# Kernel tuning notes

Measured on AMD Instinct MI355X. Metric: run time of the kernel, lower is better.

## Reference

```python
import jax, jax.numpy as jnp
import numpy as np

SIGMA = 0.01        # config['fscore_sigma']
FSCORE_W = 0.1      # config['fscore_weight']
TASK_W = 1.0        # config['task_weight']
DOMAIN_W = 0.1      # config['domain_weight']


def setup_inputs() -> dict:
    key = jax.random.key(0)
    ks = jax.random.split(key, 11)
    B, N, M, F = 8, 4096, 4096, 512
    H1, H2, D = 256, 128, 6
    return {
        "pred_pc": jax.random.normal(ks[0], (B, N, 3), jnp.float32),
        "target_pc": jax.random.normal(ks[1], (B, M, 3), jnp.float32),
        "domain_features": jax.random.normal(ks[2], (B, F), jnp.float32),
        "dataset_weights": jax.random.uniform(ks[3], (B,), jnp.float32, 0.9, 1.2),
        "W1": jax.random.normal(ks[4], (F, H1), jnp.float32) * 0.02,
        "b1": jnp.zeros((H1,), jnp.float32),
        "W2": jax.random.normal(ks[5], (H1, H2), jnp.float32) * 0.02,
        "b2": jnp.zeros((H2,), jnp.float32),
        "W3": jax.random.normal(ks[6], (H2, D), jnp.float32) * 0.02,
        "b3": jnp.zeros((D,), jnp.float32),
        "domain_labels": jax.random.randint(ks[7], (B,), 0, D),
    }


def _chamfer_mins(pred, tgt):
    # pred: [B,N,3], tgt: [B,M,3] -> squared pairwise dists [B,N,M], then dual mins
    d = (jnp.sum(pred ** 2, axis=2)[:, :, None]
         + jnp.sum(tgt ** 2, axis=2)[:, None, :]
         - 2.0 * jnp.einsum('bnd,bmd->bnm', pred, tgt))
    return jnp.min(d, axis=2), jnp.min(d, axis=1)   # [B,N], [B,M]


def reference(pred_pc, target_pc, domain_features, dataset_weights,
              W1, b1, W2, b2, W3, b3, domain_labels):
    min_a, min_b = _chamfer_mins(pred_pc, target_pc)
    c = 2.0 * SIGMA * SIGMA
    soft_a = jnp.exp(-min_a / c)
    soft_b = jnp.exp(-min_b / c)

    # batch-level task loss (compute_reconstruction_loss on full batch)
    chamfer = jnp.mean(min_a) + jnp.mean(min_b)
    prec = jnp.mean(soft_a)
    rec = jnp.mean(soft_b)
    fscore = 2.0 * prec * rec / (prec + rec + 1e-8)
    task = chamfer + FSCORE_W * (1.0 - fscore)

    # per-sample dataset-weighted loss (vectorized form of the Python loop)
    ch_i = jnp.mean(min_a, axis=1) + jnp.mean(min_b, axis=1)
    p_i = jnp.mean(soft_a, axis=1)
    r_i = jnp.mean(soft_b, axis=1)
    f_i = 2.0 * p_i * r_i / (p_i + r_i + 1e-8)
    loss_i = ch_i + FSCORE_W * (1.0 - f_i)
    dataset_weighted = jnp.mean(dataset_weights * loss_i)

    # domain loss: GRL is identity in forward; classifier in eval mode (dropout off)
    h = jax.nn.relu(domain_features @ W1 + b1)
    h = jax.nn.relu(h @ W2 + b2)
    logits = h @ W3 + b3
    logp = jax.nn.log_softmax(logits, axis=-1)
    domain = -jnp.mean(jnp.take_along_axis(logp, domain_labels[:, None], axis=1))

    total = TASK_W * task + DOMAIN_W * domain + dataset_weighted
    return total
```

## Files before the change

### kernel.cpp

```cpp
#include <hip/hip_runtime.h>
#include <math.h>

#define B 8
#define NPTS 4096
#define QPT 16
#define THREADS 256


template<int S, int LOG2S>
__global__ __launch_bounds__(THREADS, 4) void k_main(
    const float* __restrict__ pred, const float* __restrict__ targ,
    const float* __restrict__ x, const float* __restrict__ W1,
    float* __restrict__ partial, float* __restrict__ sums32,
    float* __restrict__ h1p) {
  constexpr int REFS = NPTS / S;
  int id = blockIdx.x, tid = threadIdx.x;
  __shared__ float4 sbuf4[REFS < 64 ? 64 : REFS];

  if (id >= 16 * S) {
    if (id == 16 * S + 64) {
      if (tid < 32) sums32[tid] = 0.f;
      return;
    }
    int lid = id - 16 * S;
    int b = lid >> 3, kc = lid & 7;
    float* xs = (float*)sbuf4;
    if (tid < 64) xs[tid] = x[b * 512 + kc * 64 + tid];
    __syncthreads();
    float acc = 0.f;
    const float* w = W1 + (size_t)(kc * 64) * 256 + tid;
#pragma unroll 8
    for (int k = 0; k < 64; ++k) acc = fmaf(xs[k], w[k * 256], acc);
    h1p[(b * 8 + kc) * 256 + tid] = acc;
    return;
  }

  int split = id & (S - 1);
  int b     = (id >> LOG2S) & 7;
  int dir   = id >> (LOG2S + 3);
  const float* qp = dir ? targ : pred;
  const float* rp = dir ? pred : targ;

  float4* refs = sbuf4;
  const float* rb = rp + ((size_t)b * NPTS + (size_t)split * REFS) * 3;
  for (int i = tid; i < REFS; i += THREADS) {
    float xx = rb[i * 3 + 0], yy = rb[i * 3 + 1], zz = rb[i * 3 + 2];
    refs[i] = make_float4(xx, yy, zz, 0.5f * (xx * xx + yy * yy + zz * zz));
  }
  __syncthreads();

  const float* qb = qp + (size_t)b * NPTS * 3;
  float qx[QPT], qy[QPT], qz[QPT], vmin[QPT];
#pragma unroll
  for (int i = 0; i < QPT; ++i) {
    int q = tid + i * THREADS;
    qx[i] = qb[q * 3 + 0];
    qy[i] = qb[q * 3 + 1];
    qz[i] = qb[q * 3 + 2];
    vmin[i] = 3.4e38f;
  }

  for (int j = 0; j < REFS; j += 4) {
    float4 t0 = refs[j + 0], t1 = refs[j + 1];
    float4 t2 = refs[j + 2], t3 = refs[j + 3];
    asm volatile("" : "+v"(t0.x), "+v"(t0.y), "+v"(t0.z), "+v"(t0.w),
                      "+v"(t1.x), "+v"(t1.y), "+v"(t1.z), "+v"(t1.w),
                      "+v"(t2.x), "+v"(t2.y), "+v"(t2.z), "+v"(t2.w),
                      "+v"(t3.x), "+v"(t3.y), "+v"(t3.z), "+v"(t3.w));
#pragma unroll
    for (int i = 0; i < QPT; ++i) {
      float s0 = fmaf(-qx[i], t0.x, fmaf(-qy[i], t0.y, fmaf(-qz[i], t0.z, t0.w)));
      float s1 = fmaf(-qx[i], t1.x, fmaf(-qy[i], t1.y, fmaf(-qz[i], t1.z, t1.w)));
      float s2 = fmaf(-qx[i], t2.x, fmaf(-qy[i], t2.y, fmaf(-qz[i], t2.z, t2.w)));
      float s3 = fmaf(-qx[i], t3.x, fmaf(-qy[i], t3.y, fmaf(-qz[i], t3.z, t3.w)));
      vmin[i] = fminf(fminf(vmin[i], fminf(s0, s1)), fminf(s2, s3));
    }
  }

  size_t base = (((size_t)dir * B + b) * S + split) * NPTS;
#pragma unroll
  for (int i = 0; i < QPT; ++i) {
    float qn = fmaf(qx[i], qx[i], fmaf(qy[i], qy[i], qz[i] * qz[i]));
    partial[base + tid + i * THREADS] = fmaf(2.f, vmin[i], qn);
  }
}

template<int S>
__global__ __launch_bounds__(THREADS) void k_finish(
    const float* __restrict__ partial, float* __restrict__ sums32,
    const float* __restrict__ h1p, const float* __restrict__ b1,
    const float* __restrict__ W2, const float* __restrict__ b2,
    const float* __restrict__ W3, const float* __restrict__ b3,
    const int* __restrict__ labels, float* __restrict__ nlls) {
  int id = blockIdx.x, tid = threadIdx.x;
  __shared__ float sbuf[4160];

  if (id < 64) {
    int dirb  = id >> 2;
    int chunk = id & 3;
    const float* pbase = partial + (size_t)dirb * S * NPTS
                       + (size_t)chunk * 1024 + (size_t)tid * 4;
    float4 m4 = make_float4(3.4e38f, 3.4e38f, 3.4e38f, 3.4e38f);
#pragma unroll 8
    for (int s = 0; s < S; ++s) {
      float4 v = *(const float4*)(pbase + (size_t)s * NPTS);
      m4.x = fminf(m4.x, v.x); m4.y = fminf(m4.y, v.y);
      m4.z = fminf(m4.z, v.z); m4.w = fminf(m4.w, v.w);
    }
    float s_min  = (m4.x + m4.y) + (m4.z + m4.w);
    float s_soft = (__expf(-5000.0f * m4.x) + __expf(-5000.0f * m4.y))
                 + (__expf(-5000.0f * m4.z) + __expf(-5000.0f * m4.w));
    for (int off = 32; off > 0; off >>= 1) {
      s_min  += __shfl_down(s_min,  off);
      s_soft += __shfl_down(s_soft, off);
    }
    int wave = tid >> 6, lane = tid & 63;
    if (lane == 0) { sbuf[wave * 2] = s_min; sbuf[wave * 2 + 1] = s_soft; }
    __syncthreads();
    if (tid == 0) {
      float a = 0.f, c = 0.f;
      for (int w = 0; w < 4; ++w) { a += sbuf[w * 2]; c += sbuf[w * 2 + 1]; }
      atomicAdd(&sums32[dirb * 2 + 0], a);
      atomicAdd(&sums32[dirb * 2 + 1], c);
    }
    return;
  }

  float* h1s = sbuf;
  float* pp  = sbuf + 2048;
  float* lg  = sbuf + 4096;
  for (int i = tid; i < 2048; i += THREADS) {
    int bb = i >> 8, j = i & 255;
    float a = b1[j];
#pragma unroll
    for (int kc = 0; kc < 8; ++kc) a += h1p[(bb * 8 + kc) * 256 + j];
    h1s[i] = fmaxf(a, 0.f);
  }
  __syncthreads();
  {
    int j = tid & 127, half = tid >> 7;
    float acc[8];
#pragma unroll
    for (int bb = 0; bb < 8; ++bb) acc[bb] = 0.f;
    const float* w = W2 + (size_t)(half * 128) * 128 + j;
    for (int k = 0; k < 128; ++k) {
      float wv = w[k * 128];
      int kk = half * 128 + k;
#pragma unroll
      for (int bb = 0; bb < 8; ++bb)
        acc[bb] = fmaf(h1s[bb * 256 + kk], wv, acc[bb]);
    }
#pragma unroll
    for (int bb = 0; bb < 8; ++bb) pp[(half * 8 + bb) * 128 + j] = acc[bb];
  }
  __syncthreads();
  float* h2s = sbuf;
  for (int i = tid; i < 1024; i += THREADS) {
    int bb = i >> 7, j = i & 127;
    float a = b2[j] + pp[(0 * 8 + bb) * 128 + j] + pp[(1 * 8 + bb) * 128 + j];
    h2s[i] = fmaxf(a, 0.f);
  }
  __syncthreads();
  if (tid < 48) {
    int bb = tid / 6, d = tid % 6;
    float acc = b3[d];
#pragma unroll 8
    for (int k = 0; k < 128; ++k) acc = fmaf(h2s[bb * 128 + k], W3[k * 6 + d], acc);
    lg[tid] = acc;
  }
  __syncthreads();
  if (tid < 8) {
    int bb = tid;
    float mx = lg[bb * 6];
    for (int d = 1; d < 6; ++d) mx = fmaxf(mx, lg[bb * 6 + d]);
    float se = 0.f;
    for (int d = 0; d < 6; ++d) se += __expf(lg[bb * 6 + d] - mx);
    int lab = labels[bb];
    nlls[bb] = -(lg[bb * 6 + lab] - mx - __logf(se));
  }
}

__global__ __launch_bounds__(64) void k_combine(
    const float* __restrict__ sums32, const float* __restrict__ nlls,
    const float* __restrict__ w, float* __restrict__ out) {
  if (threadIdx.x != 0) return;
  float chamfer = 0.f, prec = 0.f, rec = 0.f, dsw = 0.f, dom = 0.f;
  for (int b = 0; b < B; ++b) {
    float sa  = sums32[(0 * B + b) * 2 + 0];
    float ssa = sums32[(0 * B + b) * 2 + 1];
    float sb  = sums32[(1 * B + b) * 2 + 0];
    float ssb = sums32[(1 * B + b) * 2 + 1];
    float ma = sa / 4096.f, mb = sb / 4096.f;
    float p = ssa / 4096.f, r = ssb / 4096.f;
    chamfer += ma + mb;
    prec += p; rec += r;
    float f_i = 2.f * p * r / (p + r + 1e-8f);
    float loss_i = ma + mb + 0.1f * (1.f - f_i);
    dsw += w[b] * loss_i;
    dom += nlls[b];
  }
  chamfer *= (1.f / B); prec *= (1.f / B); rec *= (1.f / B);
  dsw *= (1.f / B); dom *= (1.f / B);
  float fscore = 2.f * prec * rec / (prec + rec + 1e-8f);
  float task = chamfer + 0.1f * (1.f - fscore);
  out[0] = 1.0f * task + 0.1f * dom + dsw;
}

template<int S, int LOG2S>
static void run_pipeline(const float* pred, const float* targ, const float* x,
                         const float* wgt, const float* W1, const float* b1,
                         const float* W2, const float* b2, const float* W3,
                         const float* b3, const int* labels, float* out,
                         char* ws, hipStream_t stream) {
  float* partial = (float*)ws;
  float* sums32  = partial + (size_t)2 * B * S * NPTS;
  float* h1p     = sums32 + 32;
  float* nlls    = h1p + 64 * 256;

  hipLaunchKernelGGL((k_main<S, LOG2S>), dim3(16 * S + 65), dim3(THREADS), 0,
                     stream, pred, targ, x, W1, partial, sums32, h1p);
  hipLaunchKernelGGL((k_finish<S>), dim3(65), dim3(THREADS), 0, stream,
                     partial, sums32, h1p, b1, W2, b2, W3, b3, labels, nlls);
  hipLaunchKernelGGL(k_combine, dim3(1), dim3(64), 0, stream,
                     sums32, nlls, wgt, out);
}

extern "C" void kernel_launch(void* const* d_in, const int* in_sizes, int n_in,
                              void* d_out, int out_size, void* d_ws, size_t ws_size,
                              hipStream_t stream) {
  const float* pred   = (const float*)d_in[0];
  const float* targ   = (const float*)d_in[1];
  const float* x      = (const float*)d_in[2];
  const float* wgt    = (const float*)d_in[3];
  const float* W1     = (const float*)d_in[4];
  const float* b1     = (const float*)d_in[5];
  const float* W2     = (const float*)d_in[6];
  const float* b2     = (const float*)d_in[7];
  const float* W3     = (const float*)d_in[8];
  const float* b3     = (const float*)d_in[9];
  const int*   labels = (const int*)d_in[10];
  float* out = (float*)d_out;
  char* ws = (char*)d_ws;

  auto need = [](int S) {
    return ((size_t)2 * B * S * NPTS + 32 + 64 * 256 + 8) * sizeof(float);
  };
  if (ws_size >= need(64))
    run_pipeline<64, 6>(pred, targ, x, wgt, W1, b1, W2, b2, W3, b3, labels,
                        out, ws, stream);
  else if (ws_size >= need(32))
    run_pipeline<32, 5>(pred, targ, x, wgt, W1, b1, W2, b2, W3, b3, labels,
                        out, ws, stream);
  else
    run_pipeline<16, 4>(pred, targ, x, wgt, W1, b1, W2, b2, W3, b3, labels,
                        out, ws, stream);
}
```

Baseline: 114.1 us.

## Pack reference pairs into SoA layout and use packed FP32 FMA

```diff
diff --git a/kernel.cpp b/kernel.cpp
--- a/kernel.cpp
+++ b/kernel.cpp
@@ -3,8 +3,11 @@
 
 #define B 8
 #define NPTS 4096
-#define QPT 16
+#define QPT 8
 #define THREADS 256
+
+typedef float v2f __attribute__((ext_vector_type(2)));
+typedef float v4f __attribute__((ext_vector_type(4)));
 
 
 template<int S, int LOG2S>
@@ -14,17 +17,18 @@
     float* __restrict__ partial, float* __restrict__ sums32,
     float* __restrict__ h1p) {
   constexpr int REFS = NPTS / S;
+  constexpr int PAIRS = REFS / 2;
   int id = blockIdx.x, tid = threadIdx.x;
-  __shared__ float4 sbuf4[REFS < 64 ? 64 : REFS];
-
-  if (id >= 16 * S) {
-    if (id == 16 * S + 64) {
+  __shared__ v4f refsP[REFS < 64 ? 64 : REFS];
+
+  if (id >= 32 * S) {
+    if (id == 32 * S + 64) {
       if (tid < 32) sums32[tid] = 0.f;
       return;
     }
-    int lid = id - 16 * S;
+    int lid = id - 32 * S;
     int b = lid >> 3, kc = lid & 7;
-    float* xs = (float*)sbuf4;
+    float* xs = (float*)refsP;
     if (tid < 64) xs[tid] = x[b * 512 + kc * 64 + tid];
     __syncthreads();
     float acc = 0.f;
@@ -35,53 +39,75 @@
     return;
   }
 
-  int split = id & (S - 1);
-  int b     = (id >> LOG2S) & 7;
-  int dir   = id >> (LOG2S + 3);
+  int split  = id & (S - 1);
+  int qchunk = (id >> LOG2S) & 1;
+  int b      = (id >> (LOG2S + 1)) & 7;
+  int dir    = id >> (LOG2S + 4);
   const float* qp = dir ? targ : pred;
   const float* rp = dir ? pred : targ;
 
-  float4* refs = sbuf4;
   const float* rb = rp + ((size_t)b * NPTS + (size_t)split * REFS) * 3;
-  for (int i = tid; i < REFS; i += THREADS) {
-    float xx = rb[i * 3 + 0], yy = rb[i * 3 + 1], zz = rb[i * 3 + 2];
-    refs[i] = make_float4(xx, yy, zz, 0.5f * (xx * xx + yy * yy + zz * zz));
+  for (int p = tid; p < PAIRS; p += THREADS) {
+    const float* r0 = rb + 6 * p;
+    float x0 = r0[0], y0 = r0[1], z0 = r0[2];
+    float x1 = r0[3], y1 = r0[4], z1 = r0[5];
+    v4f A, Bv;
+    A.x = x0; A.y = x1; A.z = y0; A.w = y1;
+    Bv.x = z0; Bv.y = z1;
+    Bv.z = 0.5f * fmaf(x0, x0, fmaf(y0, y0, z0 * z0));
+    Bv.w = 0.5f * fmaf(x1, x1, fmaf(y1, y1, z1 * z1));
+    refsP[2 * p]     = A;
+    refsP[2 * p + 1] = Bv;
   }
   __syncthreads();
 
   const float* qb = qp + (size_t)b * NPTS * 3;
-  float qx[QPT], qy[QPT], qz[QPT], vmin[QPT];
+  int q0 = qchunk * (QPT * THREADS) + tid;
+  v2f qx[QPT], qy[QPT], qz[QPT];
+  float vmin[QPT];
 #pragma unroll
   for (int i = 0; i < QPT; ++i) {
-    int q = tid + i * THREADS;
-    qx[i] = qb[q * 3 + 0];
-    qy[i] = qb[q * 3 + 1];
-    qz[i] = qb[q * 3 + 2];
+    int q = q0 + i * THREADS;
+    float xx = qb[q * 3 + 0], yy = qb[q * 3 + 1], zz = qb[q * 3 + 2];
+    qx[i].x = -xx; qx[i].y = -xx;
+    qy[i].x = -yy; qy[i].y = -yy;
+    qz[i].x = -zz; qz[i].y = -zz;
     vmin[i] = 3.4e38f;
   }
 
-  for (int j = 0; j < REFS; j += 4) {
-    float4 t0 = refs[j + 0], t1 = refs[j + 1];
-    float4 t2 = refs[j + 2], t3 = refs[j + 3];
-    asm volatile("" : "+v"(t0.x), "+v"(t0.y), "+v"(t0.z), "+v"(t0.w),
-                      "+v"(t1.x), "+v"(t1.y), "+v"(t1.z), "+v"(t1.w),
-                      "+v"(t2.x), "+v"(t2.y), "+v"(t2.z), "+v"(t2.w),
-                      "+v"(t3.x), "+v"(t3.y), "+v"(t3.z), "+v"(t3.w));
+  for (int p = 0; p < PAIRS; p += 4) {
+    v4f a0 = refsP[2 * p + 0], b0 = refsP[2 * p + 1];
+    v4f a1 = refsP[2 * p + 2], b1 = refsP[2 * p + 3];
+    v4f a2 = refsP[2 * p + 4], b2 = refsP[2 * p + 5];
+    v4f a3 = refsP[2 * p + 6], b3 = refsP[2 * p + 7];
+    asm volatile("" : "+v"(a0), "+v"(b0), "+v"(a1), "+v"(b1),
+                      "+v"(a2), "+v"(b2), "+v"(a3), "+v"(b3));
 #pragma unroll
     for (int i = 0; i < QPT; ++i) {
-      float s0 = fmaf(-qx[i], t0.x, fmaf(-qy[i], t0.y, fmaf(-qz[i], t0.z, t0.w)));
-      float s1 = fmaf(-qx[i], t1.x, fmaf(-qy[i], t1.y, fmaf(-qz[i], t1.z, t1.w)));
-      float s2 = fmaf(-qx[i], t2.x, fmaf(-qy[i], t2.y, fmaf(-qz[i], t2.z, t2.w)));
-      float s3 = fmaf(-qx[i], t3.x, fmaf(-qy[i], t3.y, fmaf(-qz[i], t3.z, t3.w)));
-      vmin[i] = fminf(fminf(vmin[i], fminf(s0, s1)), fminf(s2, s3));
+      v2f s0 = __builtin_elementwise_fma(qz[i], b0.xy, (v2f)b0.zw);
+      s0 = __builtin_elementwise_fma(qy[i], a0.zw, s0);
+      s0 = __builtin_elementwise_fma(qx[i], a0.xy, s0);
+      v2f s1 = __builtin_elementwise_fma(qz[i], b1.xy, (v2f)b1.zw);
+      s1 = __builtin_elementwise_fma(qy[i], a1.zw, s1);
+      s1 = __builtin_elementwise_fma(qx[i], a1.xy, s1);
+      v2f s2 = __builtin_elementwise_fma(qz[i], b2.xy, (v2f)b2.zw);
+      s2 = __builtin_elementwise_fma(qy[i], a2.zw, s2);
+      s2 = __builtin_elementwise_fma(qx[i], a2.xy, s2);
+      v2f s3 = __builtin_elementwise_fma(qz[i], b3.xy, (v2f)b3.zw);
+      s3 = __builtin_elementwise_fma(qy[i], a3.zw, s3);
+      s3 = __builtin_elementwise_fma(qx[i], a3.xy, s3);
+      float m0 = fminf(fminf(s0.x, s0.y), fminf(s1.x, s1.y));
+      float m1 = fminf(fminf(s2.x, s2.y), fminf(s3.x, s3.y));
+      vmin[i] = fminf(vmin[i], fminf(m0, m1));
     }
   }
 
   size_t base = (((size_t)dir * B + b) * S + split) * NPTS;
 #pragma unroll
   for (int i = 0; i < QPT; ++i) {
-    float qn = fmaf(qx[i], qx[i], fmaf(qy[i], qy[i], qz[i] * qz[i]));
-    partial[base + tid + i * THREADS] = fmaf(2.f, vmin[i], qn);
+    float xx = qx[i].x, yy = qy[i].x, zz = qz[i].x;
+    float qn = fmaf(xx, xx, fmaf(yy, yy, zz * zz));
+    partial[base + q0 + i * THREADS] = fmaf(2.f, vmin[i], qn);
   }
 }
 
@@ -217,7 +243,7 @@
   float* h1p     = sums32 + 32;
   float* nlls    = h1p + 64 * 256;
 
-  hipLaunchKernelGGL((k_main<S, LOG2S>), dim3(16 * S + 65), dim3(THREADS), 0,
+  hipLaunchKernelGGL((k_main<S, LOG2S>), dim3(32 * S + 65), dim3(THREADS), 0,
                      stream, pred, targ, x, W1, partial, sums32, h1p);
   hipLaunchKernelGGL((k_finish<S>), dim3(65), dim3(THREADS), 0, stream,
                      partial, sums32, h1p, b1, W2, b2, W3, b3, labels, nlls);
```

Result: no change. 115.5 us (+1.2%).
